# Optimization experiments

Hardware: AMD Instinct MI355X
Metric: run time of the kernel (lower is better)

The kernel has to match this reference:

```python
import jax, jax.numpy as jnp
import numpy as np

G, N, E, I, H, O = 128, 1024, 64, 128, 128, 128
EPS = 1e-5


def setup_inputs() -> dict:
    key = jax.random.key(0)
    ks = jax.random.split(key, 6)
    return {
        "feature": jax.random.normal(ks[0], (G, N, I), dtype=jnp.float32),
        "eigen": jax.random.normal(ks[1], (G, N, E), dtype=jnp.float32),
        "weights1": jax.random.normal(ks[2], (E, I, H), dtype=jnp.float32),
        "biases1": jnp.zeros((E, H), dtype=jnp.float32),
        "weights2": jax.random.normal(ks[3], (E, H, O), dtype=jnp.float32),
        "biases2": jnp.zeros((E, O), dtype=jnp.float32),
        "bn_gamma": jnp.ones((O,), dtype=jnp.float32),
        "bn_beta": jnp.zeros((O,), dtype=jnp.float32),
    }


def reference(feature, eigen, weights1, biases1, weights2, biases2, bn_gamma, bn_beta):
    # Eigen projection per graph: [G,E,I]
    spec_in = jnp.einsum('gni,gne->gei', feature, eigen)
    # Per-eigen MLP (grouped small GEMMs)
    spec_hidden = jax.nn.relu(jnp.einsum('eik,gei->gek', weights1, spec_in) + biases1)
    spec_out = jnp.einsum('eko,gek->geo', weights2, spec_hidden) + biases2
    # Inverse projection back to nodes: [G,N,O]
    h = jnp.einsum('geo,gne->gno', spec_out, eigen)
    h = h.reshape(G * N, O)
    # BatchNorm1d in training mode (biased variance over all nodes)
    mean = jnp.mean(h, axis=0)
    var = jnp.mean((h - mean) ** 2, axis=0)
    h = bn_gamma * (h - mean) * jax.lax.rsqrt(var + EPS) + bn_beta
    # Activation + residual (in_dim == out_dim)
    h = jax.nn.relu(h)
    h = feature.reshape(G * N, I) + h
    return h
```

## Files before the change

kernel.cpp:

```cpp
#include <hip/hip_runtime.h>

#define G_ 128
#define N_ 1024
#define E_ 64
#define I_ 128
#define H_ 128
#define O_ 128
#define EPSV 1e-5f

#define WS_SPECIN  0
#define WS_GRAM    4194304
#define WS_ROWSUM  6291456
#define WS_SPECOUT 6324224
#define WS_STATS   7372800
#define WS_SCALE   7373056

typedef __attribute__((ext_vector_type(4))) float f32x4;
typedef __attribute__((ext_vector_type(8))) short bf16x8;
#define MFMA16(a, b, c) __builtin_amdgcn_mfma_f32_16x16x32_bf16((a), (b), (c), 0, 0, 0)

__device__ __forceinline__ unsigned bf16_rne(float x) {
  unsigned u = __float_as_uint(x);
  return (u + 0x7fffu + ((u >> 16) & 1u)) >> 16;
}
__device__ __forceinline__ void split2(float a, float b, unsigned& hi, unsigned& lo) {
  unsigned ha = bf16_rne(a), hb = bf16_rne(b);
  float ra = a - __uint_as_float(ha << 16);
  float rb = b - __uint_as_float(hb << 16);
  hi = ha | (hb << 16);
  lo = bf16_rne(ra) | (bf16_rne(rb) << 16);
}

__global__ __launch_bounds__(256) void k1_project(
    const float* __restrict__ feature, const float* __restrict__ eigen,
    float* __restrict__ ws)
{
  __shared__ short ET[2][64][72];
  __shared__ short FT[2][128][72];
  __shared__ float rs_lds[4][64];

  const int g = blockIdx.x;
  const int s = blockIdx.y;
  const int t = threadIdx.x;
  const int l = t & 63;
  const int w = t >> 6;
  const int lm = l & 15;
  const int lk = l >> 4;
  const size_t nglob = (size_t)g * N_ + (size_t)s * 256;

  const int se = t & 63;
  const int sng = t >> 6;
  const int si = t & 127;
  const int smg = t >> 7;

  f32x4 acc[4][3];
#pragma unroll
  for (int m = 0; m < 4; ++m)
#pragma unroll
    for (int c = 0; c < 3; ++c) acc[m][c] = (f32x4){0.f, 0.f, 0.f, 0.f};

  float rs = 0.f;

  for (int ch = 0; ch < 4; ++ch) {
    __syncthreads();
    const int nb = ch * 64;

    const float* eg = eigen + (nglob + nb) * E_ + se;
#pragma unroll
    for (int p = 0; p < 4; ++p) {
      const int nl = p * 16 + sng * 4;
      float x0 = eg[(size_t)(nl + 0) * E_];
      float x1 = eg[(size_t)(nl + 1) * E_];
      float x2 = eg[(size_t)(nl + 2) * E_];
      float x3 = eg[(size_t)(nl + 3) * E_];
      rs += x0 + x1 + x2 + x3;
      unsigned h01, l01, h23, l23;
      split2(x0, x1, h01, l01);
      split2(x2, x3, h23, l23);
      const int cb = (((nl >> 3) ^ (se >> 3)) << 3) | (nl & 7);
      *(uint2*)&ET[0][se][cb] = make_uint2(h01, h23);
      *(uint2*)&ET[1][se][cb] = make_uint2(l01, l23);
    }
    const float* fg = feature + (nglob + nb) * I_ + si;
#pragma unroll
    for (int p = 0; p < 8; ++p) {
      const int nl = p * 8 + smg * 4;
      float x0 = fg[(size_t)(nl + 0) * I_];
      float x1 = fg[(size_t)(nl + 1) * I_];
      float x2 = fg[(size_t)(nl + 2) * I_];
      float x3 = fg[(size_t)(nl + 3) * I_];
      unsigned h01, l01, h23, l23;
      split2(x0, x1, h01, l01);
      split2(x2, x3, h23, l23);
      const int cb = (((nl >> 3) ^ ((si >> 3) & 7)) << 3) | (nl & 7);
      *(uint2*)&FT[0][si][cb] = make_uint2(h01, h23);
      *(uint2*)&FT[1][si][cb] = make_uint2(l01, l23);
    }
    __syncthreads();

#pragma unroll
    for (int kt = 0; kt < 2; ++kt) {
      bf16x8 ah[4], al[4];
#pragma unroll
      for (int m = 0; m < 4; ++m) {
        const int er = m * 16 + lm;
        const int cc = (((kt * 4 + lk) ^ (er >> 3)) << 3);
        ah[m] = *(const bf16x8*)&ET[0][er][cc];
        al[m] = *(const bf16x8*)&ET[1][er][cc];
      }
#pragma unroll
      for (int cl = 0; cl < 3; ++cl) {
        const int ct = w + cl * 4;
        const short(*Bh)[72] = (ct < 8) ? FT[0] : ET[0];
        const short(*Bl)[72] = (ct < 8) ? FT[1] : ET[1];
        const int br = ((ct < 8) ? ct : (ct - 8)) * 16 + lm;
        const int cc = (((kt * 4 + lk) ^ ((br >> 3) & 7)) << 3);
        bf16x8 bh = *(const bf16x8*)&Bh[br][cc];
        bf16x8 bl = *(const bf16x8*)&Bl[br][cc];
#pragma unroll
        for (int m = 0; m < 4; ++m) {
          acc[m][cl] = MFMA16(ah[m], bh, acc[m][cl]);
          acc[m][cl] = MFMA16(ah[m], bl, acc[m][cl]);
          acc[m][cl] = MFMA16(al[m], bh, acc[m][cl]);
        }
      }
    }
  }

#pragma unroll
  for (int cl = 0; cl < 3; ++cl) {
    const int ct = w + cl * 4;
#pragma unroll
    for (int m = 0; m < 4; ++m) {
#pragma unroll
      for (int r = 0; r < 4; ++r) {
        const int e = m * 16 + lk * 4 + r;
        const float v = acc[m][cl][r];
        if (ct < 8) {
          const int i = ct * 16 + lm;
          ws[WS_SPECIN + ((size_t)(s * E_ + e) * G_ + g) * I_ + i] = v;
        } else {
          const int e2 = (ct - 8) * 16 + lm;
          ws[WS_GRAM + ((size_t)(s * G_ + g) * E_ + e) * E_ + e2] = v;
        }
      }
    }
  }
  rs_lds[sng][se] = rs;
  __syncthreads();
  if (t < 64) {
    ws[WS_ROWSUM + (size_t)(s * G_ + g) * E_ + t] =
        rs_lds[0][t] + rs_lds[1][t] + rs_lds[2][t] + rs_lds[3][t];
  }
}

__global__ __launch_bounds__(256) void k2_mlp(
    const float* __restrict__ w1, const float* __restrict__ b1,
    const float* __restrict__ w2, const float* __restrict__ b2,
    float* __restrict__ ws)
{
  __shared__ float Wl[128 * 128];
  __shared__ float XT[128][32];
  __shared__ float HT[128][32];
  const int e = blockIdx.x;
  const int g0 = blockIdx.y * 32;
  const int t = threadIdx.x;
  const int tg = t >> 5;
  const int tk = t & 31;

  {
    const float4* wsrc = (const float4*)(w1 + (size_t)e * I_ * H_);
    float4* wdst = (float4*)Wl;
#pragma unroll
    for (int j = 0; j < 16; ++j) wdst[j * 256 + t] = wsrc[j * 256 + t];
  }
#pragma unroll
  for (int j = 0; j < 4; ++j) {
    int c = j * 256 + t;
    int gl = c >> 5;
    int i4 = (c & 31) * 4;
    size_t base = WS_SPECIN + ((size_t)e * G_ + g0 + gl) * I_ + i4;
    float4 v0 = *(const float4*)&ws[base];
    float4 v1 = *(const float4*)&ws[base + 1048576];
    float4 v2 = *(const float4*)&ws[base + 2097152];
    float4 v3 = *(const float4*)&ws[base + 3145728];
    XT[i4 + 0][gl] = v0.x + v1.x + v2.x + v3.x;
    XT[i4 + 1][gl] = v0.y + v1.y + v2.y + v3.y;
    XT[i4 + 2][gl] = v0.z + v1.z + v2.z + v3.z;
    XT[i4 + 3][gl] = v0.w + v1.w + v2.w + v3.w;
  }
  __syncthreads();

  {
    float4 bb = *(const float4*)&b1[e * H_ + 4 * tk];
    float h[4][4];
#pragma unroll
    for (int a = 0; a < 4; ++a) { h[a][0]=bb.x; h[a][1]=bb.y; h[a][2]=bb.z; h[a][3]=bb.w; }
    for (int i = 0; i < 128; ++i) {
      float4 xv = *(const float4*)&XT[i][4 * tg];
      float4 wr = *(const float4*)&Wl[i * 128 + 4 * tk];
      float xa[4] = {xv.x, xv.y, xv.z, xv.w};
      float wv[4] = {wr.x, wr.y, wr.z, wr.w};
#pragma unroll
      for (int a = 0; a < 4; ++a)
#pragma unroll
        for (int b = 0; b < 4; ++b) h[a][b] = fmaf(xa[a], wv[b], h[a][b]);
    }
#pragma unroll
    for (int a = 0; a < 4; ++a)
#pragma unroll
      for (int b = 0; b < 4; ++b)
        HT[4 * tk + b][4 * tg + a] = fmaxf(h[a][b], 0.f);
  }
  __syncthreads();
  {
    const float4* wsrc = (const float4*)(w2 + (size_t)e * H_ * O_);
    float4* wdst = (float4*)Wl;
#pragma unroll
    for (int j = 0; j < 16; ++j) wdst[j * 256 + t] = wsrc[j * 256 + t];
  }
  __syncthreads();
  {
    float4 bb = *(const float4*)&b2[e * O_ + 4 * tk];
    float o[4][4];
#pragma unroll
    for (int a = 0; a < 4; ++a) { o[a][0]=bb.x; o[a][1]=bb.y; o[a][2]=bb.z; o[a][3]=bb.w; }
    for (int k = 0; k < 128; ++k) {
      float4 hv = *(const float4*)&HT[k][4 * tg];
      float4 wr = *(const float4*)&Wl[k * 128 + 4 * tk];
      float ha[4] = {hv.x, hv.y, hv.z, hv.w};
      float wv[4] = {wr.x, wr.y, wr.z, wr.w};
#pragma unroll
      for (int a = 0; a < 4; ++a)
#pragma unroll
        for (int b = 0; b < 4; ++b) o[a][b] = fmaf(ha[a], wv[b], o[a][b]);
    }
#pragma unroll
    for (int a = 0; a < 4; ++a) {
      size_t ob = WS_SPECOUT + ((size_t)(g0 + 4 * tg + a) * E_ + e) * O_ + 4 * tk;
      *(float4*)&ws[ob] = make_float4(o[a][0], o[a][1], o[a][2], o[a][3]);
    }
  }
}

__global__ __launch_bounds__(256) void k2b_stats(float* __restrict__ ws)
{
  __shared__ float So[64][64];
  __shared__ float Gm[64][64];
  __shared__ float Rsh[64];
  __shared__ float RedM[16][64];
  __shared__ float RedS[16][64];
  const int g = blockIdx.x;
  const int oc = blockIdx.y;
  const int t = threadIdx.x;
  const int tr = t >> 4;
  const int tc = t & 15;

#pragma unroll
  for (int j = 0; j < 4; ++j) {
    int c = j * 256 + t;
    int e = c >> 4;
    int o4 = (c & 15) * 4;
    *(float4*)&So[e][o4] = *(const float4*)&ws[WS_SPECOUT + (size_t)g * E_ * O_ +
                                               (size_t)e * O_ + oc * 64 + o4];
  }
#pragma unroll
  for (int j = 0; j < 4; ++j) {
    int c = j * 256 + t;
    size_t base = WS_GRAM + (size_t)g * 4096 + (size_t)c * 4;
    float4 v0 = *(const float4*)&ws[base];
    float4 v1 = *(const float4*)&ws[base + 524288];
    float4 v2 = *(const float4*)&ws[base + 1048576];
    float4 v3 = *(const float4*)&ws[base + 1572864];
    float4 r;
    r.x = v0.x + v1.x + v2.x + v3.x;
    r.y = v0.y + v1.y + v2.y + v3.y;
    r.z = v0.z + v1.z + v2.z + v3.z;
    r.w = v0.w + v1.w + v2.w + v3.w;
    ((float4*)(&Gm[0][0]))[c] = r;
  }
  if (t < 64) {
    Rsh[t] = ws[WS_ROWSUM + (size_t)g * E_ + t]
           + ws[WS_ROWSUM + 8192 + (size_t)g * E_ + t]
           + ws[WS_ROWSUM + 16384 + (size_t)g * E_ + t]
           + ws[WS_ROWSUM + 24576 + (size_t)g * E_ + t];
  }
  __syncthreads();

  float y[4][4];
#pragma unroll
  for (int a = 0; a < 4; ++a)
#pragma unroll
    for (int b = 0; b < 4; ++b) y[a][b] = 0.f;

  for (int e2 = 0; e2 < 64; ++e2) {
    float4 gv = *(const float4*)&Gm[e2][4 * tr];
    float4 sv = *(const float4*)&So[e2][4 * tc];
    float ga[4] = {gv.x, gv.y, gv.z, gv.w};
    float sb[4] = {sv.x, sv.y, sv.z, sv.w};
#pragma unroll
    for (int a = 0; a < 4; ++a)
#pragma unroll
      for (int b = 0; b < 4; ++b) y[a][b] = fmaf(ga[a], sb[b], y[a][b]);
  }

  float sp[4] = {0.f, 0.f, 0.f, 0.f};
  float sm[4] = {0.f, 0.f, 0.f, 0.f};
#pragma unroll
  for (int a = 0; a < 4; ++a) {
    const int e1 = 4 * tr + a;
    float4 sv = *(const float4*)&So[e1][4 * tc];
    float r = Rsh[e1];
    float sb[4] = {sv.x, sv.y, sv.z, sv.w};
#pragma unroll
    for (int b = 0; b < 4; ++b) {
      sp[b] = fmaf(sb[b], y[a][b], sp[b]);
      sm[b] = fmaf(sb[b], r, sm[b]);
    }
  }
  *(float4*)&RedS[tr][4 * tc] = make_float4(sp[0], sp[1], sp[2], sp[3]);
  *(float4*)&RedM[tr][4 * tc] = make_float4(sm[0], sm[1], sm[2], sm[3]);
  __syncthreads();
  if (t < 64) {
    float ssq = 0.f, smm = 0.f;
#pragma unroll
    for (int wv = 0; wv < 16; ++wv) { ssq += RedS[wv][t]; smm += RedM[wv][t]; }
    atomicAdd(&ws[WS_STATS + oc * 64 + t], smm);
    atomicAdd(&ws[WS_STATS + 128 + oc * 64 + t], ssq);
  }
}

__global__ void k2c_finalize(const float* __restrict__ gamma, const float* __restrict__ beta,
                             float* __restrict__ ws)
{
  const int t = threadIdx.x;
  if (t < 128) {
    const float inv = 1.f / (float)(G_ * N_);
    float mean = ws[WS_STATS + t] * inv;
    float var = fmaxf(ws[WS_STATS + 128 + t] * inv - mean * mean, 0.f);
    float sc = gamma[t] * rsqrtf(var + EPSV);
    ws[WS_SCALE + t] = sc;
    ws[WS_SCALE + 128 + t] = beta[t] - mean * sc;
  }
}

__global__ __launch_bounds__(256) void k3_output(
    const float* __restrict__ feature, const float* __restrict__ eigen,
    const float* __restrict__ ws, float* __restrict__ out)
{
  __shared__ float Al[64][68];
  __shared__ float Bl[64][128];
  const int g = blockIdx.x;
  const int nb = blockIdx.y * 64;
  const int t = threadIdx.x;
  const int tr = t >> 4;
  const int tc = t & 15;

  {
    const float4* asrc = (const float4*)(eigen + ((size_t)g * N_ + nb) * E_);
#pragma unroll
    for (int j = 0; j < 4; ++j) {
      int c = j * 256 + t;
      *(float4*)&Al[c >> 4][(c & 15) * 4] = asrc[c];
    }
    const float4* bsrc = (const float4*)(ws + WS_SPECOUT + (size_t)g * E_ * O_);
    float4* bdst = (float4*)(&Bl[0][0]);
#pragma unroll
    for (int j = 0; j < 8; ++j) bdst[j * 256 + t] = bsrc[j * 256 + t];
  }
  __syncthreads();

  float acc[4][8];
#pragma unroll
  for (int a = 0; a < 4; ++a)
#pragma unroll
    for (int b = 0; b < 8; ++b) acc[a][b] = 0.f;

  for (int kq = 0; kq < 16; ++kq) {
    const int k0 = 4 * kq;
    float4 a0 = *(const float4*)&Al[tr][k0];
    float4 a1 = *(const float4*)&Al[16 + tr][k0];
    float4 a2 = *(const float4*)&Al[32 + tr][k0];
    float4 a3 = *(const float4*)&Al[48 + tr][k0];
    float am[4][4] = {{a0.x, a0.y, a0.z, a0.w},
                      {a1.x, a1.y, a1.z, a1.w},
                      {a2.x, a2.y, a2.z, a2.w},
                      {a3.x, a3.y, a3.z, a3.w}};
#pragma unroll
    for (int kk = 0; kk < 4; ++kk) {
      float4 bx = *(const float4*)&Bl[k0 + kk][4 * tc];
      float4 by = *(const float4*)&Bl[k0 + kk][64 + 4 * tc];
#pragma unroll
      for (int r = 0; r < 4; ++r) {
        float av = am[r][kk];
        acc[r][0] = fmaf(av, bx.x, acc[r][0]);
        acc[r][1] = fmaf(av, bx.y, acc[r][1]);
        acc[r][2] = fmaf(av, bx.z, acc[r][2]);
        acc[r][3] = fmaf(av, bx.w, acc[r][3]);
        acc[r][4] = fmaf(av, by.x, acc[r][4]);
        acc[r][5] = fmaf(av, by.y, acc[r][5]);
        acc[r][6] = fmaf(av, by.z, acc[r][6]);
        acc[r][7] = fmaf(av, by.w, acc[r][7]);
      }
    }
  }

  float4 sca = *(const float4*)&ws[WS_SCALE + 4 * tc];
  float4 scb = *(const float4*)&ws[WS_SCALE + 64 + 4 * tc];
  float4 sha = *(const float4*)&ws[WS_SCALE + 128 + 4 * tc];
  float4 shb = *(const float4*)&ws[WS_SCALE + 128 + 64 + 4 * tc];
#pragma unroll
  for (int r = 0; r < 4; ++r) {
    const size_t row = (size_t)g * N_ + nb + 16 * r + tr;
    const float* fp = feature + row * I_;
    float* op = out + row * O_;
    float4 f1 = *(const float4*)&fp[4 * tc];
    float4 f2 = *(const float4*)&fp[64 + 4 * tc];
    float4 o1, o2;
    o1.x = f1.x + fmaxf(fmaf(acc[r][0], sca.x, sha.x), 0.f);
    o1.y = f1.y + fmaxf(fmaf(acc[r][1], sca.y, sha.y), 0.f);
    o1.z = f1.z + fmaxf(fmaf(acc[r][2], sca.z, sha.z), 0.f);
    o1.w = f1.w + fmaxf(fmaf(acc[r][3], sca.w, sha.w), 0.f);
    o2.x = f2.x + fmaxf(fmaf(acc[r][4], scb.x, shb.x), 0.f);
    o2.y = f2.y + fmaxf(fmaf(acc[r][5], scb.y, shb.y), 0.f);
    o2.z = f2.z + fmaxf(fmaf(acc[r][6], scb.z, shb.z), 0.f);
    o2.w = f2.w + fmaxf(fmaf(acc[r][7], scb.w, shb.w), 0.f);
    *(float4*)&op[4 * tc] = o1;
    *(float4*)&op[64 + 4 * tc] = o2;
  }
}

extern "C" void kernel_launch(void* const* d_in, const int* in_sizes, int n_in,
                              void* d_out, int out_size, void* d_ws, size_t ws_size,
                              hipStream_t stream) {
  (void)in_sizes; (void)n_in; (void)out_size; (void)ws_size;
  const float* feature = (const float*)d_in[0];
  const float* eigen   = (const float*)d_in[1];
  const float* w1      = (const float*)d_in[2];
  const float* b1      = (const float*)d_in[3];
  const float* w2      = (const float*)d_in[4];
  const float* b2      = (const float*)d_in[5];
  const float* gamma   = (const float*)d_in[6];
  const float* beta    = (const float*)d_in[7];
  float* out = (float*)d_out;
  float* ws  = (float*)d_ws;

  hipMemsetAsync(ws + WS_STATS, 0, 256 * sizeof(float), stream);
  k1_project<<<dim3(G_, 4), 256, 0, stream>>>(feature, eigen, ws);
  k2_mlp<<<dim3(E_, 4), 256, 0, stream>>>(w1, b1, w2, b2, ws);
  k2b_stats<<<dim3(G_, 2), 256, 0, stream>>>(ws);
  k2c_finalize<<<1, 128, 0, stream>>>(gamma, beta, ws);
  k3_output<<<dim3(G_, N_ / 64), 256, 0, stream>>>(feature, eigen, ws, out);
}
```

Before: 229.1 us.

## Split projection over feature halves, stream MLP weights, use split-bf16 MFMA in output

```diff
diff --git a/kernel.cpp b/kernel.cpp
--- a/kernel.cpp
+++ b/kernel.cpp
@@ -36,11 +36,12 @@
     float* __restrict__ ws)
 {
   __shared__ short ET[2][64][72];
-  __shared__ short FT[2][128][72];
+  __shared__ short FT[2][64][72];
   __shared__ float rs_lds[4][64];
 
   const int g = blockIdx.x;
   const int s = blockIdx.y;
+  const int cb = blockIdx.z;
   const int t = threadIdx.x;
   const int l = t & 63;
   const int w = t >> 6;
@@ -50,15 +51,13 @@
 
   const int se = t & 63;
   const int sng = t >> 6;
-  const int si = t & 127;
-  const int smg = t >> 7;
-
-  f32x4 acc[4][3];
-#pragma unroll
-  for (int m = 0; m < 4; ++m)
-#pragma unroll
-    for (int c = 0; c < 3; ++c) acc[m][c] = (f32x4){0.f, 0.f, 0.f, 0.f};
-
+
+  f32x4 acc[4][2];
+#pragma unroll
+  for (int m = 0; m < 4; ++m) {
+    acc[m][0] = (f32x4){0.f, 0.f, 0.f, 0.f};
+    acc[m][1] = (f32x4){0.f, 0.f, 0.f, 0.f};
+  }
   float rs = 0.f;
 
   for (int ch = 0; ch < 4; ++ch) {
@@ -77,14 +76,14 @@
       unsigned h01, l01, h23, l23;
       split2(x0, x1, h01, l01);
       split2(x2, x3, h23, l23);
-      const int cb = (((nl >> 3) ^ (se >> 3)) << 3) | (nl & 7);
-      *(uint2*)&ET[0][se][cb] = make_uint2(h01, h23);
-      *(uint2*)&ET[1][se][cb] = make_uint2(l01, l23);
-    }
-    const float* fg = feature + (nglob + nb) * I_ + si;
-#pragma unroll
-    for (int p = 0; p < 8; ++p) {
-      const int nl = p * 8 + smg * 4;
+      const int cc = (((nl >> 3) ^ (se >> 3)) << 3) | (nl & 7);
+      *(uint2*)&ET[0][se][cc] = make_uint2(h01, h23);
+      *(uint2*)&ET[1][se][cc] = make_uint2(l01, l23);
+    }
+    const float* fg = feature + (nglob + nb) * I_ + cb * 64 + se;
+#pragma unroll
+    for (int p = 0; p < 4; ++p) {
+      const int nl = p * 16 + sng * 4;
       float x0 = fg[(size_t)(nl + 0) * I_];
       float x1 = fg[(size_t)(nl + 1) * I_];
       float x2 = fg[(size_t)(nl + 2) * I_];
@@ -92,9 +91,9 @@
       unsigned h01, l01, h23, l23;
       split2(x0, x1, h01, l01);
       split2(x2, x3, h23, l23);
-      const int cb = (((nl >> 3) ^ ((si >> 3) & 7)) << 3) | (nl & 7);
-      *(uint2*)&FT[0][si][cb] = make_uint2(h01, h23);
-      *(uint2*)&FT[1][si][cb] = make_uint2(l01, l23);
+      const int cc = (((nl >> 3) ^ (se >> 3)) << 3) | (nl & 7);
+      *(uint2*)&FT[0][se][cc] = make_uint2(h01, h23);
+      *(uint2*)&FT[1][se][cc] = make_uint2(l01, l23);
     }
     __syncthreads();
 
@@ -108,49 +107,51 @@
         ah[m] = *(const bf16x8*)&ET[0][er][cc];
         al[m] = *(const bf16x8*)&ET[1][er][cc];
       }
-#pragma unroll
-      for (int cl = 0; cl < 3; ++cl) {
-        const int ct = w + cl * 4;
-        const short(*Bh)[72] = (ct < 8) ? FT[0] : ET[0];
-        const short(*Bl)[72] = (ct < 8) ? FT[1] : ET[1];
-        const int br = ((ct < 8) ? ct : (ct - 8)) * 16 + lm;
-        const int cc = (((kt * 4 + lk) ^ ((br >> 3) & 7)) << 3);
-        bf16x8 bh = *(const bf16x8*)&Bh[br][cc];
-        bf16x8 bl = *(const bf16x8*)&Bl[br][cc];
+      const int br = w * 16 + lm;
+      const int cc = (((kt * 4 + lk) ^ (br >> 3)) << 3);
+      {
+        bf16x8 bh = *(const bf16x8*)&FT[0][br][cc];
+        bf16x8 bl = *(const bf16x8*)&FT[1][br][cc];
 #pragma unroll
         for (int m = 0; m < 4; ++m) {
-          acc[m][cl] = MFMA16(ah[m], bh, acc[m][cl]);
-          acc[m][cl] = MFMA16(ah[m], bl, acc[m][cl]);
-          acc[m][cl] = MFMA16(al[m], bh, acc[m][cl]);
+          acc[m][0] = MFMA16(ah[m], bh, acc[m][0]);
+          acc[m][0] = MFMA16(ah[m], bl, acc[m][0]);
+          acc[m][0] = MFMA16(al[m], bh, acc[m][0]);
         }
       }
-    }
-  }
-
-#pragma unroll
-  for (int cl = 0; cl < 3; ++cl) {
-    const int ct = w + cl * 4;
-#pragma unroll
-    for (int m = 0; m < 4; ++m) {
-#pragma unroll
-      for (int r = 0; r < 4; ++r) {
-        const int e = m * 16 + lk * 4 + r;
-        const float v = acc[m][cl][r];
-        if (ct < 8) {
-          const int i = ct * 16 + lm;
-          ws[WS_SPECIN + ((size_t)(s * E_ + e) * G_ + g) * I_ + i] = v;
-        } else {
-          const int e2 = (ct - 8) * 16 + lm;
-          ws[WS_GRAM + ((size_t)(s * G_ + g) * E_ + e) * E_ + e2] = v;
+      if (cb == 0) {
+        bf16x8 bh = *(const bf16x8*)&ET[0][br][cc];
+        bf16x8 bl = *(const bf16x8*)&ET[1][br][cc];
+#pragma unroll
+        for (int m = 0; m < 4; ++m) {
+          acc[m][1] = MFMA16(ah[m], bh, acc[m][1]);
+          acc[m][1] = MFMA16(ah[m], bl, acc[m][1]);
+          acc[m][1] = MFMA16(al[m], bh, acc[m][1]);
         }
       }
     }
   }
-  rs_lds[sng][se] = rs;
-  __syncthreads();
-  if (t < 64) {
-    ws[WS_ROWSUM + (size_t)(s * G_ + g) * E_ + t] =
-        rs_lds[0][t] + rs_lds[1][t] + rs_lds[2][t] + rs_lds[3][t];
+
+#pragma unroll
+  for (int m = 0; m < 4; ++m) {
+#pragma unroll
+    for (int r = 0; r < 4; ++r) {
+      const int e = m * 16 + lk * 4 + r;
+      const int i = cb * 64 + w * 16 + lm;
+      ws[WS_SPECIN + ((size_t)(s * E_ + e) * G_ + g) * I_ + i] = acc[m][0][r];
+      if (cb == 0) {
+        const int e2 = w * 16 + lm;
+        ws[WS_GRAM + ((size_t)(s * G_ + g) * E_ + e) * E_ + e2] = acc[m][1][r];
+      }
+    }
+  }
+  if (cb == 0) {
+    rs_lds[sng][se] = rs;
+    __syncthreads();
+    if (t < 64) {
+      ws[WS_ROWSUM + (size_t)(s * G_ + g) * E_ + t] =
+          rs_lds[0][t] + rs_lds[1][t] + rs_lds[2][t] + rs_lds[3][t];
+    }
   }
 }
 
@@ -159,26 +160,19 @@
     const float* __restrict__ w2, const float* __restrict__ b2,
     float* __restrict__ ws)
 {
-  __shared__ float Wl[128 * 128];
-  __shared__ float XT[128][32];
-  __shared__ float HT[128][32];
+  __shared__ float XT[128][17];
+  __shared__ float HT[128][17];
   const int e = blockIdx.x;
-  const int g0 = blockIdx.y * 32;
+  const int g0 = blockIdx.y * 16;
   const int t = threadIdx.x;
   const int tg = t >> 5;
   const int tk = t & 31;
 
-  {
-    const float4* wsrc = (const float4*)(w1 + (size_t)e * I_ * H_);
-    float4* wdst = (float4*)Wl;
-#pragma unroll
-    for (int j = 0; j < 16; ++j) wdst[j * 256 + t] = wsrc[j * 256 + t];
-  }
-#pragma unroll
-  for (int j = 0; j < 4; ++j) {
-    int c = j * 256 + t;
-    int gl = c >> 5;
-    int i4 = (c & 31) * 4;
+#pragma unroll
+  for (int j = 0; j < 2; ++j) {
+    int idx = j * 256 + t;
+    int gl = idx >> 5;
+    int i4 = (idx & 31) * 4;
     size_t base = WS_SPECIN + ((size_t)e * G_ + g0 + gl) * I_ + i4;
     float4 v0 = *(const float4*)&ws[base];
     float4 v1 = *(const float4*)&ws[base + 1048576];
@@ -192,52 +186,53 @@
   __syncthreads();
 
   {
+    const float* w1e = w1 + (size_t)e * I_ * H_;
     float4 bb = *(const float4*)&b1[e * H_ + 4 * tk];
-    float h[4][4];
-#pragma unroll
-    for (int a = 0; a < 4; ++a) { h[a][0]=bb.x; h[a][1]=bb.y; h[a][2]=bb.z; h[a][3]=bb.w; }
+    float h[2][4];
+#pragma unroll
+    for (int a = 0; a < 2; ++a) { h[a][0]=bb.x; h[a][1]=bb.y; h[a][2]=bb.z; h[a][3]=bb.w; }
     for (int i = 0; i < 128; ++i) {
-      float4 xv = *(const float4*)&XT[i][4 * tg];
-      float4 wr = *(const float4*)&Wl[i * 128 + 4 * tk];
-      float xa[4] = {xv.x, xv.y, xv.z, xv.w};
-      float wv[4] = {wr.x, wr.y, wr.z, wr.w};
-#pragma unroll
-      for (int a = 0; a < 4; ++a)
-#pragma unroll
-        for (int b = 0; b < 4; ++b) h[a][b] = fmaf(xa[a], wv[b], h[a][b]);
-    }
-#pragma unroll
-    for (int a = 0; a < 4; ++a)
+      float4 wr = *(const float4*)&w1e[(size_t)i * H_ + 4 * tk];
+      float xa0 = XT[i][2 * tg];
+      float xa1 = XT[i][2 * tg + 1];
+      h[0][0] = fmaf(xa0, wr.x, h[0][0]);
+      h[0][1] = fmaf(xa0, wr.y, h[0][1]);
+      h[0][2] = fmaf(xa0, wr.z, h[0][2]);
+      h[0][3] = fmaf(xa0, wr.w, h[0][3]);
+      h[1][0] = fmaf(xa1, wr.x, h[1][0]);
+      h[1][1] = fmaf(xa1, wr.y, h[1][1]);
+      h[1][2] = fmaf(xa1, wr.z, h[1][2]);
+      h[1][3] = fmaf(xa1, wr.w, h[1][3]);
+    }
+#pragma unroll
+    for (int a = 0; a < 2; ++a)
 #pragma unroll
       for (int b = 0; b < 4; ++b)
-        HT[4 * tk + b][4 * tg + a] = fmaxf(h[a][b], 0.f);
+        HT[4 * tk + b][2 * tg + a] = fmaxf(h[a][b], 0.f);
   }
   __syncthreads();
   {
-    const float4* wsrc = (const float4*)(w2 + (size_t)e * H_ * O_);
-    float4* wdst = (float4*)Wl;
-#pragma unroll
-    for (int j = 0; j < 16; ++j) wdst[j * 256 + t] = wsrc[j * 256 + t];
-  }
-  __syncthreads();
-  {
+    const float* w2e = w2 + (size_t)e * H_ * O_;
     float4 bb = *(const float4*)&b2[e * O_ + 4 * tk];
-    float o[4][4];
-#pragma unroll
-    for (int a = 0; a < 4; ++a) { o[a][0]=bb.x; o[a][1]=bb.y; o[a][2]=bb.z; o[a][3]=bb.w; }
+    float o[2][4];
+#pragma unroll
+    for (int a = 0; a < 2; ++a) { o[a][0]=bb.x; o[a][1]=bb.y; o[a][2]=bb.z; o[a][3]=bb.w; }
     for (int k = 0; k < 128; ++k) {
-      float4 hv = *(const float4*)&HT[k][4 * tg];
-      float4 wr = *(const float4*)&Wl[k * 128 + 4 * tk];
-      float ha[4] = {hv.x, hv.y, hv.z, hv.w};
-      float wv[4] = {wr.x, wr.y, wr.z, wr.w};
-#pragma unroll
-      for (int a = 0; a < 4; ++a)
-#pragma unroll
-        for (int b = 0; b < 4; ++b) o[a][b] = fmaf(ha[a], wv[b], o[a][b]);
-    }
-#pragma unroll
-    for (int a = 0; a < 4; ++a) {
-      size_t ob = WS_SPECOUT + ((size_t)(g0 + 4 * tg + a) * E_ + e) * O_ + 4 * tk;
+      float4 wr = *(const float4*)&w2e[(size_t)k * O_ + 4 * tk];
+      float ha0 = HT[k][2 * tg];
+      float ha1 = HT[k][2 * tg + 1];
+      o[0][0] = fmaf(ha0, wr.x, o[0][0]);
+      o[0][1] = fmaf(ha0, wr.y, o[0][1]);
+      o[0][2] = fmaf(ha0, wr.z, o[0][2]);
+      o[0][3] = fmaf(ha0, wr.w, o[0][3]);
+      o[1][0] = fmaf(ha1, wr.x, o[1][0]);
+      o[1][1] = fmaf(ha1, wr.y, o[1][1]);
+      o[1][2] = fmaf(ha1, wr.z, o[1][2]);
+      o[1][3] = fmaf(ha1, wr.w, o[1][3]);
+    }
+#pragma unroll
+    for (int a = 0; a < 2; ++a) {
+      size_t ob = WS_SPECOUT + ((size_t)(g0 + 2 * tg + a) * E_ + e) * O_ + 4 * tk;
       *(float4*)&ws[ob] = make_float4(o[a][0], o[a][1], o[a][2], o[a][3]);
     }
   }
@@ -348,85 +343,95 @@
     const float* __restrict__ feature, const float* __restrict__ eigen,
     const float* __restrict__ ws, float* __restrict__ out)
 {
-  __shared__ float Al[64][68];
-  __shared__ float Bl[64][128];
+  __shared__ short AL[2][128][64];
   const int g = blockIdx.x;
-  const int nb = blockIdx.y * 64;
+  const int nb = blockIdx.y * 128;
   const int t = threadIdx.x;
-  const int tr = t >> 4;
-  const int tc = t & 15;
+  const int l = t & 63;
+  const int w = t >> 6;
+  const int lm = l & 15;
+  const int lk = l >> 4;
+
+  char* A0 = (char*)&AL[0][0][0];
+  char* A1 = (char*)&AL[1][0][0];
 
   {
-    const float4* asrc = (const float4*)(eigen + ((size_t)g * N_ + nb) * E_);
-#pragma unroll
-    for (int j = 0; j < 4; ++j) {
-      int c = j * 256 + t;
-      *(float4*)&Al[c >> 4][(c & 15) * 4] = asrc[c];
-    }
-    const float4* bsrc = (const float4*)(ws + WS_SPECOUT + (size_t)g * E_ * O_);
-    float4* bdst = (float4*)(&Bl[0][0]);
-#pragma unroll
-    for (int j = 0; j < 8; ++j) bdst[j * 256 + t] = bsrc[j * 256 + t];
+    const float* eg = eigen + ((size_t)g * N_ + nb) * E_;
+#pragma unroll
+    for (int j = 0; j < 8; ++j) {
+      int idx = j * 256 + t;
+      int n = idx >> 4;
+      int e4 = (idx & 15) * 4;
+      float4 v = *(const float4*)&eg[(size_t)n * E_ + e4];
+      unsigned h01, l01, h23, l23;
+      split2(v.x, v.y, h01, l01);
+      split2(v.z, v.w, h23, l23);
+      int off = (n * 128 + e4 * 2) ^ ((n & 7) << 4);
+      *(uint2*)(A0 + off) = make_uint2(h01, h23);
+      *(uint2*)(A1 + off) = make_uint2(l01, l23);
+    }
+  }
+
+  bf16x8 bh[2][2], bl[2][2];
+  float sc[2], sh[2];
+  {
+    const float* so = ws + WS_SPECOUT + (size_t)g * E_ * O_;
+#pragma unroll
+    for (int oti = 0; oti < 2; ++oti) {
+      const int o = (2 * w + oti) * 16 + lm;
+      sc[oti] = ws[WS_SCALE + o];
+      sh[oti] = ws[WS_SCALE + 128 + o];
+#pragma unroll
+      for (int kt = 0; kt < 2; ++kt) {
+#pragma unroll
+        for (int j = 0; j < 8; ++j) {
+          float x = so[(size_t)(kt * 32 + lk * 8 + j) * O_ + o];
+          unsigned hb = bf16_rne(x);
+          float r = x - __uint_as_float(hb << 16);
+          bh[oti][kt][j] = (short)hb;
+          bl[oti][kt][j] = (short)bf16_rne(r);
+        }
+      }
+    }
   }
   __syncthreads();
 
-  float acc[4][8];
-#pragma unroll
-  for (int a = 0; a < 4; ++a)
-#pragma unroll
-    for (int b = 0; b < 8; ++b) acc[a][b] = 0.f;
-
-  for (int kq = 0; kq < 16; ++kq) {
-    const int k0 = 4 * kq;
-    float4 a0 = *(const float4*)&Al[tr][k0];
-    float4 a1 = *(const float4*)&Al[16 + tr][k0];
-    float4 a2 = *(const float4*)&Al[32 + tr][k0];
-    float4 a3 = *(const float4*)&Al[48 + tr][k0];
-    float am[4][4] = {{a0.x, a0.y, a0.z, a0.w},
-                      {a1.x, a1.y, a1.z, a1.w},
-                      {a2.x, a2.y, a2.z, a2.w},
-                      {a3.x, a3.y, a3.z, a3.w}};
-#pragma unroll
-    for (int kk = 0; kk < 4; ++kk) {
-      float4 bx = *(const float4*)&Bl[k0 + kk][4 * tc];
-      float4 by = *(const float4*)&Bl[k0 + kk][64 + 4 * tc];
+  f32x4 acc[8][2];
+#pragma unroll
+  for (int nt = 0; nt < 8; ++nt) {
+    acc[nt][0] = (f32x4){0.f, 0.f, 0.f, 0.f};
+    acc[nt][1] = (f32x4){0.f, 0.f, 0.f, 0.f};
+  }
+
+#pragma unroll
+  for (int kt = 0; kt < 2; ++kt) {
+#pragma unroll
+    for (int nt = 0; nt < 8; ++nt) {
+      const int n = nt * 16 + lm;
+      const int off = (n * 128 + kt * 64 + lk * 16) ^ ((n & 7) << 4);
+      bf16x8 ah = *(const bf16x8*)(A0 + off);
+      bf16x8 al2 = *(const bf16x8*)(A1 + off);
+#pragma unroll
+      for (int oti = 0; oti < 2; ++oti) {
+        acc[nt][oti] = MFMA16(ah, bh[oti][kt], acc[nt][oti]);
+        acc[nt][oti] = MFMA16(ah, bl[oti][kt], acc[nt][oti]);
+        acc[nt][oti] = MFMA16(al2, bh[oti][kt], acc[nt][oti]);
+      }
+    }
+  }
+
+#pragma unroll
+  for (int nt = 0; nt < 8; ++nt) {
+#pragma unroll
+    for (int oti = 0; oti < 2; ++oti) {
+      const int o = (2 * w + oti) * 16 + lm;
 #pragma unroll
       for (int r = 0; r < 4; ++r) {
-        float av = am[r][kk];
-        acc[r][0] = fmaf(av, bx.x, acc[r][0]);
-        acc[r][1] = fmaf(av, bx.y, acc[r][1]);
-        acc[r][2] = fmaf(av, bx.z, acc[r][2]);
-        acc[r][3] = fmaf(av, bx.w, acc[r][3]);
-        acc[r][4] = fmaf(av, by.x, acc[r][4]);
-        acc[r][5] = fmaf(av, by.y, acc[r][5]);
-        acc[r][6] = fmaf(av, by.z, acc[r][6]);
-        acc[r][7] = fmaf(av, by.w, acc[r][7]);
-      }
-    }
-  }
-
-  float4 sca = *(const float4*)&ws[WS_SCALE + 4 * tc];
-  float4 scb = *(const float4*)&ws[WS_SCALE + 64 + 4 * tc];
-  float4 sha = *(const float4*)&ws[WS_SCALE + 128 + 4 * tc];
-  float4 shb = *(const float4*)&ws[WS_SCALE + 128 + 64 + 4 * tc];
-#pragma unroll
-  for (int r = 0; r < 4; ++r) {
-    const size_t row = (size_t)g * N_ + nb + 16 * r + tr;
-    const float* fp = feature + row * I_;
-    float* op = out + row * O_;
-    float4 f1 = *(const float4*)&fp[4 * tc];
-    float4 f2 = *(const float4*)&fp[64 + 4 * tc];
-    float4 o1, o2;
-    o1.x = f1.x + fmaxf(fmaf(acc[r][0], sca.x, sha.x), 0.f);
-    o1.y = f1.y + fmaxf(fmaf(acc[r][1], sca.y, sha.y), 0.f);
-    o1.z = f1.z + fmaxf(fmaf(acc[r][2], sca.z, sha.z), 0.f);
-    o1.w = f1.w + fmaxf(fmaf(acc[r][3], sca.w, sha.w), 0.f);
-    o2.x = f2.x + fmaxf(fmaf(acc[r][4], scb.x, shb.x), 0.f);
-    o2.y = f2.y + fmaxf(fmaf(acc[r][5], scb.y, shb.y), 0.f);
-    o2.z = f2.z + fmaxf(fmaf(acc[r][6], scb.z, shb.z), 0.f);
-    o2.w = f2.w + fmaxf(fmaf(acc[r][7], scb.w, shb.w), 0.f);
-    *(float4*)&op[4 * tc] = o1;
-    *(float4*)&op[64 + 4 * tc] = o2;
+        const size_t grow = (size_t)g * N_ + nb + nt * 16 + lk * 4 + r;
+        float hv = fmaxf(fmaf(acc[nt][oti][r], sc[oti], sh[oti]), 0.f);
+        out[grow * O_ + o] = feature[grow * I_ + o] + hv;
+      }
+    }
   }
 }
 
@@ -446,9 +451,9 @@
   float* ws  = (float*)d_ws;
 
   hipMemsetAsync(ws + WS_STATS, 0, 256 * sizeof(float), stream);
-  k1_project<<<dim3(G_, 4), 256, 0, stream>>>(feature, eigen, ws);
-  k2_mlp<<<dim3(E_, 4), 256, 0, stream>>>(w1, b1, w2, b2, ws);
+  k1_project<<<dim3(G_, 4, 2), 256, 0, stream>>>(feature, eigen, ws);
+  k2_mlp<<<dim3(E_, 8), 256, 0, stream>>>(w1, b1, w2, b2, ws);
   k2b_stats<<<dim3(G_, 2), 256, 0, stream>>>(ws);
   k2c_finalize<<<1, 128, 0, stream>>>(gamma, beta, ws);
-  k3_output<<<dim3(G_, N_ / 64), 256, 0, stream>>>(feature, eigen, ws, out);
-}
+  k3_output<<<dim3(G_, N_ / 128), 256, 0, stream>>>(feature, eigen, ws, out);
+}
```

Measured after the change: 224.1 us. 1.02x faster.
